# Performance work log

Measured on AMD Instinct MI355X. Metric: run time of the kernel, lower is better.

## Reference

```python
import jax, jax.numpy as jnp
import numpy as np

N = 65536      # n query/support points
NN = 34        # neighbors per point
K = 15         # kernel points
IN_F = 64
OUT_F = 64
RADIUS = 2.5
KP_EXTENT_CFG = 1.0
DENSITY = 5.0
EXTENT = KP_EXTENT_CFG * RADIUS / DENSITY  # effective KP_extent = 0.5
BN_EPS = 1e-6
LRELU_SLOPE = 0.1
POINT_DIM = 4  # modulated=True -> 3 offset dims + 1 modulation per kernel point


def make_kernel_points():
    # Deterministic stand-in for the precomputed kernel dispositions loaded
    # from disk in KPConv (fixed='center': first point at origin). Points lie
    # inside a ball of radius 1.5 * extent.
    rng = np.random.RandomState(42)
    kp = rng.normal(size=(K, 3))
    kp /= np.linalg.norm(kp, axis=1, keepdims=True)
    kp *= rng.uniform(0.3, 1.0, size=(K, 1))
    kp[0] = 0.0
    return jnp.asarray(kp * (1.5 * EXTENT), dtype=jnp.float32)


def setup_inputs() -> dict:
    key = jax.random.key(0)
    ks = jax.random.split(key, 8)
    query_points = jax.random.uniform(ks[0], (N, 3), dtype=jnp.float32)
    support_points = jax.random.uniform(ks[1], (N, 3), dtype=jnp.float32)
    neighbors_indices = jax.random.randint(ks[2], (N, NN), 0, N, dtype=jnp.int32)
    features = jax.random.normal(ks[3], (N, IN_F), dtype=jnp.float32)
    # weight_variable: truncated normal with std sqrt(2/size[-1])
    weight = jax.random.truncated_normal(ks[4], -2.0, 2.0, (K, IN_F, OUT_F), jnp.float32) * np.sqrt(2.0 / OUT_F)
    off_dim = POINT_DIM * K
    offset_weight = jax.random.truncated_normal(ks[5], -2.0, 2.0, (K, IN_F, off_dim), jnp.float32) * np.sqrt(2.0 / off_dim)
    offset_bias = jnp.zeros((off_dim,), jnp.float32)
    bn_gamma = jnp.ones((OUT_F,), jnp.float32)
    bn_beta = jnp.zeros((OUT_F,), jnp.float32)
    kernel_points = make_kernel_points()
    return dict(query_points=query_points, support_points=support_points,
                neighbors_indices=neighbors_indices, features=features,
                weight=weight, offset_weight=offset_weight, offset_bias=offset_bias,
                bn_gamma=bn_gamma, bn_beta=bn_beta, kernel_points=kernel_points)


def _influence(sq_dist):
    # KP_influence='linear': relu(1 - d / extent)
    return jax.nn.relu(1.0 - jnp.sqrt(sq_dist) / EXTENT)


def reference(query_points, support_points, neighbors_indices, features,
              weight, offset_weight, offset_bias, bn_gamma, bn_beta, kernel_points):
    n = query_points.shape[0]
    # Shadow point (far away) / shadow feature (zeros) appended at index n0
    supp_pad = jnp.concatenate([support_points, jnp.full((1, 3), 1e6, jnp.float32)], 0)
    feat_pad = jnp.concatenate([features, jnp.zeros((1, IN_F), jnp.float32)], 0)

    neigh_pts = supp_pad[neighbors_indices] - query_points[:, None, :]   # [n,nn,3]
    neigh_feats = feat_pad[neighbors_indices]                            # [n,nn,in]

    # ---- rigid KPConv producing per-point offsets (+ modulations) ----
    sq0 = jnp.sum((neigh_pts[:, :, None, :] - kernel_points[None, None]) ** 2, -1)  # [n,nn,K]
    w0 = _influence(sq0)
    wf0 = jnp.einsum('nak,nac->nkc', w0, neigh_feats)                    # [n,K,in]
    f0 = jnp.einsum('nkc,kcd->nd', wf0, offset_weight) + offset_bias     # [n,4K]
    offsets = f0[:, :3 * K].reshape(n, K, 3) * EXTENT                    # rescale to layer extent
    modulations = 2.0 * jax.nn.sigmoid(f0[:, 3 * K:])                    # [n,K]

    # ---- deformable KPConv ----
    def_kp = kernel_points[None] + offsets                               # [n,K,3]
    sq = jnp.sum((neigh_pts[:, :, None, :] - def_kp[:, None, :, :]) ** 2, -1)  # [n,nn,K]
    w = _influence(sq)                                                   # aggregation_mode='sum'
    wf = jnp.einsum('nak,nac->nkc', w, neigh_feats) * modulations[:, :, None]
    x = jnp.einsum('nkc,kco->no', wf, weight)                            # [n,out]

    # BatchNorm1d (training-mode batch stats, eps=1e-6) + LeakyReLU(0.1)
    mean = x.mean(0)
    var = x.var(0)
    x = (x - mean) * jax.lax.rsqrt(var + BN_EPS) * bn_gamma + bn_beta
    return jnp.where(x >= 0, x, LRELU_SLOPE * x)
```

## Files before the change

### kernel.cpp

```cpp
#include <hip/hip_runtime.h>
#include <math.h>

#define NPTS 65536

using half8   = __attribute__((ext_vector_type(8))) _Float16;
using half4   = __attribute__((ext_vector_type(4))) _Float16;
using floatx4 = __attribute__((ext_vector_type(4))) float;

__global__ __launch_bounds__(256) void k_prep(
    const float* __restrict__ ow, const float* __restrict__ w,
    const float* __restrict__ feat,
    _Float16* __restrict__ owt, _Float16* __restrict__ wt,
    _Float16* __restrict__ featH)
{
  int b = blockIdx.x;
  if (b < 256) {
    int i = b * 256 + threadIdx.x;
    int d = i >> 10, kc = i & 1023, c = kc >> 4, k = kc & 15;
    owt[i] = (k < 15 && d < 60) ? (_Float16)ow[(k * 64 + c) * 60 + d] : (_Float16)0.f;
    wt[i]  = (k < 15) ? (_Float16)w[(k * 64 + c) * 64 + d] : (_Float16)0.f;
  } else {
    int j = (b - 256) * 256 + threadIdx.x;
    float4 f = ((const float4*)feat)[j];
    half4 h = {(_Float16)f.x, (_Float16)f.y, (_Float16)f.z, (_Float16)f.w};
    ((half4*)featH)[j] = h;
  }
}

__global__ __launch_bounds__(256, 3) void k_fused(
    const float* __restrict__ query, const float* __restrict__ support,
    const int* __restrict__ nidx, const _Float16* __restrict__ featH,
    const float* __restrict__ kpts, const float* __restrict__ obias,
    const _Float16* __restrict__ owt, const _Float16* __restrict__ wt,
    float* __restrict__ outx)
{
  __shared__ float                  npx[16][34], npy[16][34], npz[16][34];
  __shared__ unsigned short         sidx[16][34];
  __shared__ __align__(16) _Float16 fT[4][64 * 32];
  __shared__ unsigned int           fx2[4][64];
  __shared__ __align__(16) _Float16 wfh[16 * 520];
  __shared__ float                  dk[16][64];

  const int tid  = threadIdx.x;
  const int wave = tid >> 6, lane = tid & 63;
  const int quad = lane >> 4, mm = lane & 15;
  const int base = blockIdx.x * 16;
  _Float16* fTw = fT[wave];
  unsigned int* fTw32 = (unsigned int*)fTw;
  unsigned int* fx2w = fx2[wave];
  const floatx4 fz = {0.f, 0.f, 0.f, 0.f};
  const int me = (mm < 15) ? mm : 14;

  for (int s = tid; s < 544; s += 256) {
    int pt = s / 34, a = s - pt * 34;
    int n = base + pt;
    int id = nidx[n * 34 + a];
    npx[pt][a] = support[id * 3 + 0] - query[n * 3 + 0];
    npy[pt][a] = support[id * 3 + 1] - query[n * 3 + 1];
    npz[pt][a] = support[id * 3 + 2] - query[n * 3 + 2];
    sidx[pt][a] = (unsigned short)id;
  }
  __syncthreads();

  auto load_g = [&](int pl, uint4* g0, uint4* g1) {
    #pragma unroll
    for (int it = 0; it < 3; ++it) {
      int task = it * 64 + lane;
      if (task < 136) {
        int rp = task >> 3, ch = task & 7;
        int i0 = (int)sidx[pl][2 * rp], i1 = (int)sidx[pl][2 * rp + 1];
        g0[it] = *(const uint4*)(featH + i0 * 64 + ch * 8);
        g1[it] = *(const uint4*)(featH + i1 * 64 + ch * 8);
      }
    }
  };
  auto transpose_g = [&](const uint4* g0, const uint4* g1) {
    #pragma unroll
    for (int it = 0; it < 3; ++it) {
      int task = it * 64 + lane;
      if (task < 136) {
        int rp = task >> 3, ch = task & 7;
        const uint* p0 = (const uint*)&g0[it];
        const uint* p1 = (const uint*)&g1[it];
        if (rp < 16) {
          int chunk = rp >> 2, o = rp & 3;
          #pragma unroll
          for (int cc = 0; cc < 8; ++cc) {
            int c  = ch * 8 + cc;
            int pc = chunk ^ ((ch ^ cc) & 3);
            uint v = __builtin_amdgcn_perm(p1[cc >> 1], p0[cc >> 1],
                                           (cc & 1) ? 0x07060302u : 0x05040100u);
            fTw32[c * 16 + pc * 4 + o] = v;
          }
        } else {
          #pragma unroll
          for (int cc = 0; cc < 8; ++cc) {
            uint v = __builtin_amdgcn_perm(p1[cc >> 1], p0[cc >> 1],
                                           (cc & 1) ? 0x07060302u : 0x05040100u);
            fx2w[ch * 8 + cc] = v;
          }
        }
      }
    }
  };

  auto conv_point = [&](int pl, float kx, float ky, float kz, const float* md,
                        floatx4* hold) {
    half8 a0;
    #pragma unroll
    for (int j = 0; j < 8; ++j) {
      int a = quad * 8 + j;
      float dx = npx[pl][a] - kx, dy = npy[pl][a] - ky, dz = npz[pl][a] - kz;
      float wv = 1.f - 2.f * sqrtf(dx * dx + dy * dy + dz * dz);
      a0[j] = (_Float16)fmaxf(wv, 0.f);
    }
    float w32, w33;
    {
      float dx = npx[pl][32] - kx, dy = npy[pl][32] - ky, dz = npz[pl][32] - kz;
      w32 = fmaxf(1.f - 2.f * sqrtf(dx * dx + dy * dy + dz * dz), 0.f);
      dx = npx[pl][33] - kx; dy = npy[pl][33] - ky; dz = npz[pl][33] - kz;
      w33 = fmaxf(1.f - 2.f * sqrtf(dx * dx + dy * dy + dz * dz), 0.f);
    }
    float w32r[4], w33r[4];
    #pragma unroll
    for (int r = 0; r < 4; ++r) {
      int src = (quad * 4 + r) << 2;
      w32r[r] = __int_as_float(__builtin_amdgcn_ds_bpermute(src, __float_as_int(w32)));
      w33r[r] = __int_as_float(__builtin_amdgcn_ds_bpermute(src, __float_as_int(w33)));
    }

    floatx4 acc[4];
    #pragma unroll
    for (int ct = 0; ct < 4; ++ct) {
      int c  = ct * 16 + mm;
      int pc = quad ^ (((c >> 3) ^ c) & 3);
      half8 b = *(const half8*)(fTw + c * 32 + pc * 8);
      acc[ct] = __builtin_amdgcn_mfma_f32_16x16x32_f16(a0, b, fz, 0, 0, 0);
    }
    #pragma unroll
    for (int ct = 0; ct < 4; ++ct) {
      int c = ct * 16 + mm;
      uint fp = fx2w[c];
      _Float16 lo = __builtin_bit_cast(_Float16, (unsigned short)(fp & 0xffffu));
      _Float16 hi = __builtin_bit_cast(_Float16, (unsigned short)(fp >> 16));
      float flo = (float)lo, fhi = (float)hi;
      #pragma unroll
      for (int r = 0; r < 4; ++r)
        acc[ct][r] = (acc[ct][r] + w32r[r] * flo + w33r[r] * fhi) * md[r];
    }

    _Float16* wp = wfh + pl * 520;
    #pragma unroll
    for (int ct = 0; ct < 2; ++ct) {
      half4 h = {(_Float16)acc[ct][0], (_Float16)acc[ct][1],
                 (_Float16)acc[ct][2], (_Float16)acc[ct][3]};
      *(half4*)(wp + (ct * 16 + mm) * 16 + quad * 4) = h;
    }
    hold[0] = acc[2]; hold[1] = acc[3];
  };

  auto write_hold = [&](const floatx4 (*hold)[2]) {
    #pragma unroll
    for (int pp = 0; pp < 4; ++pp) {
      _Float16* wp = wfh + (wave * 4 + pp) * 520;
      #pragma unroll
      for (int ct = 0; ct < 2; ++ct) {
        const floatx4& a = hold[pp][ct];
        half4 h = {(_Float16)a[0], (_Float16)a[1], (_Float16)a[2], (_Float16)a[3]};
        *(half4*)(wp + (ct * 16 + mm) * 16 + quad * 4) = h;
      }
    }
  };

  auto gemm_half = [&](const _Float16* bmat, int koff, floatx4& A, floatx4& B) {
    const _Float16* brow = bmat + (wave * 16 + mm) * 1024 + koff;
    const _Float16* arow = wfh + mm * 520;
    #pragma unroll
    for (int k2 = 0; k2 < 16; ++k2) {
      half8 af = *(const half8*)(arow + k2 * 32 + quad * 8);
      half8 bf = *(const half8*)(brow + k2 * 32 + quad * 8);
      if (k2 & 1) B = __builtin_amdgcn_mfma_f32_16x16x32_f16(af, bf, B, 0, 0, 0);
      else        A = __builtin_amdgcn_mfma_f32_16x16x32_f16(af, bf, A, 0, 0, 0);
    }
  };

  uint4 G0[2][3], G1[2][3];
  floatx4 hold[4][2];
  const float one4[4] = {1.f, 1.f, 1.f, 1.f};

  {
    float k0x = kpts[me * 3 + 0], k0y = kpts[me * 3 + 1], k0z = kpts[me * 3 + 2];
    load_g(wave * 4, G0[0], G1[0]);
    #pragma unroll
    for (int pp = 0; pp < 4; ++pp) {
      int pl = wave * 4 + pp;
      if (pp < 3) load_g(pl + 1, G0[(pp + 1) & 1], G1[(pp + 1) & 1]);
      transpose_g(G0[pp & 1], G1[pp & 1]);
      conv_point(pl, k0x, k0y, k0z, one4, hold[pp]);
    }
  }
  load_g(wave * 4, G0[0], G1[0]);
  __syncthreads();

  {
    floatx4 A = fz, B = fz;
    gemm_half(owt, 0, A, B);
    __syncthreads();
    write_hold(hold);
    __syncthreads();
    gemm_half(owt, 512, A, B);
    int d = wave * 16 + mm;
    float bv = (d < 60) ? obias[d] : 0.f;
    float kv = (d < 45) ? kpts[d] : 0.f;
    #pragma unroll
    for (int r = 0; r < 4; ++r) {
      int pt = quad * 4 + r;
      float v = A[r] + B[r] + bv;
      float o = (d < 45) ? (kv + 0.5f * v)
                         : (2.f / (1.f + expf(-v)));
      dk[pt][d] = o;
    }
  }
  __syncthreads();

  #pragma unroll
  for (int pp = 0; pp < 4; ++pp) {
    int pl = wave * 4 + pp;
    if (pp < 3) load_g(pl + 1, G0[(pp + 1) & 1], G1[(pp + 1) & 1]);
    float kx = dk[pl][me * 3 + 0], ky = dk[pl][me * 3 + 1], kz = dk[pl][me * 3 + 2];
    float md[4];
    #pragma unroll
    for (int r = 0; r < 4; ++r) {
      int k = quad * 4 + r;
      md[r] = (k < 15) ? dk[pl][45 + k] : 1.f;
    }
    transpose_g(G0[pp & 1], G1[pp & 1]);
    conv_point(pl, kx, ky, kz, md, hold[pp]);
  }
  __syncthreads();

  {
    floatx4 A = fz, B = fz;
    gemm_half(wt, 0, A, B);
    __syncthreads();
    write_hold(hold);
    __syncthreads();
    gemm_half(wt, 512, A, B);
    int d = wave * 16 + mm;
    #pragma unroll
    for (int r = 0; r < 4; ++r)
      outx[(base + quad * 4 + r) * 64 + d] = A[r] + B[r];
  }
}

__global__ __launch_bounds__(256) void k_stats(
    const float* __restrict__ x, float* __restrict__ stats)
{
  __shared__ float red[512];
  const int tid = threadIdx.x;
  const int c = tid & 63, g = tid >> 6;
  float s1 = 0.f, s2 = 0.f;
  for (int r = blockIdx.x * 4 + g; r < NPTS; r += 1024) {
    float v = x[r * 64 + c];
    s1 += v; s2 += v * v;
  }
  red[tid] = s1; red[256 + tid] = s2;
  __syncthreads();
  if (tid < 64) {
    s1 = red[tid] + red[tid + 64] + red[tid + 128] + red[tid + 192];
    s2 = red[256 + tid] + red[256 + tid + 64] + red[256 + tid + 128] + red[256 + tid + 192];
    atomicAdd(&stats[c], s1);
    atomicAdd(&stats[64 + c], s2);
  }
}

__global__ __launch_bounds__(256) void k_norm(
    float* __restrict__ x, const float* __restrict__ stats,
    const float* __restrict__ gamma, const float* __restrict__ beta)
{
  const int i = blockIdx.x * 256 + threadIdx.x;
  float4 v = ((float4*)x)[i];
  const int c0 = (i * 4) & 63;
  float o[4] = {v.x, v.y, v.z, v.w};
  #pragma unroll
  for (int j = 0; j < 4; ++j) {
    int c = c0 + j;
    float mean = stats[c] * (1.f / NPTS);
    float var  = stats[64 + c] * (1.f / NPTS) - mean * mean;
    float s = rsqrtf(var + 1e-6f) * gamma[c];
    float y = (o[j] - mean) * s + beta[c];
    o[j] = (y >= 0.f) ? y : 0.1f * y;
  }
  float4 rv = {o[0], o[1], o[2], o[3]};
  ((float4*)x)[i] = rv;
}

extern "C" void kernel_launch(void* const* d_in, const int* in_sizes, int n_in,
                              void* d_out, int out_size, void* d_ws, size_t ws_size,
                              hipStream_t stream)
{
  const float* query   = (const float*)d_in[0];
  const float* support = (const float*)d_in[1];
  const int*   nidx    = (const int*)d_in[2];
  const float* feat    = (const float*)d_in[3];
  const float* weight  = (const float*)d_in[4];
  const float* oweight = (const float*)d_in[5];
  const float* obias   = (const float*)d_in[6];
  const float* gamma   = (const float*)d_in[7];
  const float* beta    = (const float*)d_in[8];
  const float* kpts    = (const float*)d_in[9];
  float* x = (float*)d_out;

  char* ws = (char*)d_ws;
  _Float16* featH = (_Float16*)ws;
  _Float16* owt   = (_Float16*)(ws + 8388608);
  _Float16* wt    = (_Float16*)(ws + 8519680);
  float*    stats = (float*)(ws + 8650752);

  hipMemsetAsync(stats, 0, 512, stream);
  k_prep<<<4352, 256, 0, stream>>>(oweight, weight, feat, owt, wt, featH);
  k_fused<<<4096, 256, 0, stream>>>(query, support, nidx, featH, kpts, obias,
                                    owt, wt, x);
  k_stats<<<256, 256, 0, stream>>>(x, stats);
  k_norm<<<4096, 256, 0, stream>>>(x, stats, gamma, beta);
}
```

Before: 306.7 us.

## Shrink LDS staging to quarter tiles, fuse BN stats into main kernel

The weighted-feature staging buffer drops from half to quarter K-chunks, so the two GEMMs run in four stages and more accumulators are held in registers. LDS use falls, allowing launch bounds of 4 blocks per CU instead of 3. Neighbor offsets are packed as float4 with a precomputed squared norm, so distances come from a dot-product expansion. The fT layout is reswizzled. The separate stats kernel is removed: each block reduces its column sums with shuffles and adds them atomically, which costs more atomics and extra barriers.

```diff
diff --git a/kernel.cpp b/kernel.cpp
--- a/kernel.cpp
+++ b/kernel.cpp
@@ -27,19 +27,19 @@
   }
 }
 
-__global__ __launch_bounds__(256, 3) void k_fused(
+__global__ __launch_bounds__(256, 4) void k_fused(
     const float* __restrict__ query, const float* __restrict__ support,
     const int* __restrict__ nidx, const _Float16* __restrict__ featH,
     const float* __restrict__ kpts, const float* __restrict__ obias,
     const _Float16* __restrict__ owt, const _Float16* __restrict__ wt,
-    float* __restrict__ outx)
+    float* __restrict__ outx, float* __restrict__ stats)
 {
-  __shared__ float                  npx[16][34], npy[16][34], npz[16][34];
+  __shared__ float4                 np4[16][34];
   __shared__ unsigned short         sidx[16][34];
   __shared__ __align__(16) _Float16 fT[4][64 * 32];
   __shared__ unsigned int           fx2[4][64];
-  __shared__ __align__(16) _Float16 wfh[16 * 520];
-  __shared__ float                  dk[16][64];
+  __shared__ __align__(16) _Float16 wfh[16 * 264];
+  __shared__ float                  dk[16][60];
 
   const int tid  = threadIdx.x;
   const int wave = tid >> 6, lane = tid & 63;
@@ -55,9 +55,11 @@
     int pt = s / 34, a = s - pt * 34;
     int n = base + pt;
     int id = nidx[n * 34 + a];
-    npx[pt][a] = support[id * 3 + 0] - query[n * 3 + 0];
-    npy[pt][a] = support[id * 3 + 1] - query[n * 3 + 1];
-    npz[pt][a] = support[id * 3 + 2] - query[n * 3 + 2];
+    float dx = support[id * 3 + 0] - query[n * 3 + 0];
+    float dy = support[id * 3 + 1] - query[n * 3 + 1];
+    float dz = support[id * 3 + 2] - query[n * 3 + 2];
+    float4 q = {dx, dy, dz, dx * dx + dy * dy + dz * dz};
+    np4[pt][a] = q;
     sidx[pt][a] = (unsigned short)id;
   }
   __syncthreads();
@@ -87,10 +89,11 @@
           #pragma unroll
           for (int cc = 0; cc < 8; ++cc) {
             int c  = ch * 8 + cc;
-            int pc = chunk ^ ((ch ^ cc) & 3);
+            int f  = ((c & 7) << 3) | (c >> 3);
+            int pc = chunk ^ (((c >> 3) ^ c) & 3);
             uint v = __builtin_amdgcn_perm(p1[cc >> 1], p0[cc >> 1],
                                            (cc & 1) ? 0x07060302u : 0x05040100u);
-            fTw32[c * 16 + pc * 4 + o] = v;
+            fTw32[f * 16 + pc * 4 + o] = v;
           }
         } else {
           #pragma unroll
@@ -105,21 +108,26 @@
   };
 
   auto conv_point = [&](int pl, float kx, float ky, float kz, const float* md,
-                        floatx4* hold) {
+                        floatx4* hold3) {
+    float hk = kx * kx + ky * ky + kz * kz;
     half8 a0;
     #pragma unroll
     for (int j = 0; j < 8; ++j) {
       int a = quad * 8 + j;
-      float dx = npx[pl][a] - kx, dy = npy[pl][a] - ky, dz = npz[pl][a] - kz;
-      float wv = 1.f - 2.f * sqrtf(dx * dx + dy * dy + dz * dz);
+      float4 q = np4[pl][a];
+      float dt = q.x * kx + q.y * ky + q.z * kz;
+      float d2 = fmaxf(q.w + hk - 2.f * dt, 0.f);
+      float wv = 1.f - 2.f * sqrtf(d2);
       a0[j] = (_Float16)fmaxf(wv, 0.f);
     }
     float w32, w33;
     {
-      float dx = npx[pl][32] - kx, dy = npy[pl][32] - ky, dz = npz[pl][32] - kz;
-      w32 = fmaxf(1.f - 2.f * sqrtf(dx * dx + dy * dy + dz * dz), 0.f);
-      dx = npx[pl][33] - kx; dy = npy[pl][33] - ky; dz = npz[pl][33] - kz;
-      w33 = fmaxf(1.f - 2.f * sqrtf(dx * dx + dy * dy + dz * dz), 0.f);
+      float4 q = np4[pl][32];
+      float dt = q.x * kx + q.y * ky + q.z * kz;
+      w32 = fmaxf(1.f - 2.f * sqrtf(fmaxf(q.w + hk - 2.f * dt, 0.f)), 0.f);
+      q = np4[pl][33];
+      dt = q.x * kx + q.y * ky + q.z * kz;
+      w33 = fmaxf(1.f - 2.f * sqrtf(fmaxf(q.w + hk - 2.f * dt, 0.f)), 0.f);
     }
     float w32r[4], w33r[4];
     #pragma unroll
@@ -133,8 +141,9 @@
     #pragma unroll
     for (int ct = 0; ct < 4; ++ct) {
       int c  = ct * 16 + mm;
+      int f  = ((c & 7) << 3) | (c >> 3);
       int pc = quad ^ (((c >> 3) ^ c) & 3);
-      half8 b = *(const half8*)(fTw + c * 32 + pc * 8);
+      half8 b = *(const half8*)(fTw + f * 32 + pc * 8);
       acc[ct] = __builtin_amdgcn_mfma_f32_16x16x32_f16(a0, b, fz, 0, 0, 0);
     }
     #pragma unroll
@@ -149,34 +158,27 @@
         acc[ct][r] = (acc[ct][r] + w32r[r] * flo + w33r[r] * fhi) * md[r];
     }
 
-    _Float16* wp = wfh + pl * 520;
-    #pragma unroll
-    for (int ct = 0; ct < 2; ++ct) {
-      half4 h = {(_Float16)acc[ct][0], (_Float16)acc[ct][1],
-                 (_Float16)acc[ct][2], (_Float16)acc[ct][3]};
-      *(half4*)(wp + (ct * 16 + mm) * 16 + quad * 4) = h;
-    }
-    hold[0] = acc[2]; hold[1] = acc[3];
-  };
-
-  auto write_hold = [&](const floatx4 (*hold)[2]) {
+    _Float16* wp = wfh + pl * 264;
+    half4 h = {(_Float16)acc[0][0], (_Float16)acc[0][1],
+               (_Float16)acc[0][2], (_Float16)acc[0][3]};
+    *(half4*)(wp + mm * 16 + quad * 4) = h;
+    hold3[0] = acc[1]; hold3[1] = acc[2]; hold3[2] = acc[3];
+  };
+
+  auto write_hold = [&](const floatx4 (*hold)[3], int idx) {
     #pragma unroll
     for (int pp = 0; pp < 4; ++pp) {
-      _Float16* wp = wfh + (wave * 4 + pp) * 520;
-      #pragma unroll
-      for (int ct = 0; ct < 2; ++ct) {
-        const floatx4& a = hold[pp][ct];
-        half4 h = {(_Float16)a[0], (_Float16)a[1], (_Float16)a[2], (_Float16)a[3]};
-        *(half4*)(wp + (ct * 16 + mm) * 16 + quad * 4) = h;
-      }
-    }
-  };
-
-  auto gemm_half = [&](const _Float16* bmat, int koff, floatx4& A, floatx4& B) {
-    const _Float16* brow = bmat + (wave * 16 + mm) * 1024 + koff;
-    const _Float16* arow = wfh + mm * 520;
-    #pragma unroll
-    for (int k2 = 0; k2 < 16; ++k2) {
+      const floatx4& a = hold[pp][idx];
+      half4 h = {(_Float16)a[0], (_Float16)a[1], (_Float16)a[2], (_Float16)a[3]};
+      *(half4*)(wfh + (wave * 4 + pp) * 264 + mm * 16 + quad * 4) = h;
+    }
+  };
+
+  auto gemm_q = [&](const _Float16* bmat, int p, floatx4& A, floatx4& B) {
+    const _Float16* brow = bmat + (wave * 16 + mm) * 1024 + p * 256;
+    const _Float16* arow = wfh + mm * 264;
+    #pragma unroll
+    for (int k2 = 0; k2 < 8; ++k2) {
       half8 af = *(const half8*)(arow + k2 * 32 + quad * 8);
       half8 bf = *(const half8*)(brow + k2 * 32 + quad * 8);
       if (k2 & 1) B = __builtin_amdgcn_mfma_f32_16x16x32_f16(af, bf, B, 0, 0, 0);
@@ -185,7 +187,7 @@
   };
 
   uint4 G0[2][3], G1[2][3];
-  floatx4 hold[4][2];
+  floatx4 hold[4][3];
   const float one4[4] = {1.f, 1.f, 1.f, 1.f};
 
   {
@@ -204,11 +206,13 @@
 
   {
     floatx4 A = fz, B = fz;
-    gemm_half(owt, 0, A, B);
-    __syncthreads();
-    write_hold(hold);
-    __syncthreads();
-    gemm_half(owt, 512, A, B);
+    gemm_q(owt, 0, A, B);
+    __syncthreads(); write_hold(hold, 0); __syncthreads();
+    gemm_q(owt, 1, A, B);
+    __syncthreads(); write_hold(hold, 1); __syncthreads();
+    gemm_q(owt, 2, A, B);
+    __syncthreads(); write_hold(hold, 2); __syncthreads();
+    gemm_q(owt, 3, A, B);
     int d = wave * 16 + mm;
     float bv = (d < 60) ? obias[d] : 0.f;
     float kv = (d < 45) ? kpts[d] : 0.f;
@@ -216,9 +220,9 @@
     for (int r = 0; r < 4; ++r) {
       int pt = quad * 4 + r;
       float v = A[r] + B[r] + bv;
-      float o = (d < 45) ? (kv + 0.5f * v)
-                         : (2.f / (1.f + expf(-v)));
-      dk[pt][d] = o;
+      if (d < 60)
+        dk[pt][d] = (d < 45) ? (kv + 0.5f * v)
+                             : (2.f / (1.f + expf(-v)));
     }
   }
   __syncthreads();
@@ -232,7 +236,9 @@
     #pragma unroll
     for (int r = 0; r < 4; ++r) {
       int k = quad * 4 + r;
-      md[r] = (k < 15) ? dk[pl][45 + k] : 1.f;
+      int kk = (k < 15) ? k : 14;
+      float t = dk[pl][45 + kk];
+      md[r] = (k < 15) ? t : 1.f;
     }
     transpose_g(G0[pp & 1], G1[pp & 1]);
     conv_point(pl, kx, ky, kz, md, hold[pp]);
@@ -241,36 +247,27 @@
 
   {
     floatx4 A = fz, B = fz;
-    gemm_half(wt, 0, A, B);
-    __syncthreads();
-    write_hold(hold);
-    __syncthreads();
-    gemm_half(wt, 512, A, B);
+    gemm_q(wt, 0, A, B);
+    __syncthreads(); write_hold(hold, 0); __syncthreads();
+    gemm_q(wt, 1, A, B);
+    __syncthreads(); write_hold(hold, 1); __syncthreads();
+    gemm_q(wt, 2, A, B);
+    __syncthreads(); write_hold(hold, 2); __syncthreads();
+    gemm_q(wt, 3, A, B);
     int d = wave * 16 + mm;
-    #pragma unroll
-    for (int r = 0; r < 4; ++r)
-      outx[(base + quad * 4 + r) * 64 + d] = A[r] + B[r];
-  }
-}
-
-__global__ __launch_bounds__(256) void k_stats(
-    const float* __restrict__ x, float* __restrict__ stats)
-{
-  __shared__ float red[512];
-  const int tid = threadIdx.x;
-  const int c = tid & 63, g = tid >> 6;
-  float s1 = 0.f, s2 = 0.f;
-  for (int r = blockIdx.x * 4 + g; r < NPTS; r += 1024) {
-    float v = x[r * 64 + c];
-    s1 += v; s2 += v * v;
-  }
-  red[tid] = s1; red[256 + tid] = s2;
-  __syncthreads();
-  if (tid < 64) {
-    s1 = red[tid] + red[tid + 64] + red[tid + 128] + red[tid + 192];
-    s2 = red[256 + tid] + red[256 + tid + 64] + red[256 + tid + 128] + red[256 + tid + 192];
-    atomicAdd(&stats[c], s1);
-    atomicAdd(&stats[64 + c], s2);
+    float s1 = 0.f, s2 = 0.f;
+    #pragma unroll
+    for (int r = 0; r < 4; ++r) {
+      float v = A[r] + B[r];
+      outx[(base + quad * 4 + r) * 64 + d] = v;
+      s1 += v; s2 += v * v;
+    }
+    s1 += __shfl_xor(s1, 16); s2 += __shfl_xor(s2, 16);
+    s1 += __shfl_xor(s1, 32); s2 += __shfl_xor(s2, 32);
+    if (lane < 16) {
+      atomicAdd(&stats[d], s1);
+      atomicAdd(&stats[64 + d], s2);
+    }
   }
 }
 
@@ -320,7 +317,6 @@
   hipMemsetAsync(stats, 0, 512, stream);
   k_prep<<<4352, 256, 0, stream>>>(oweight, weight, feat, owt, wt, featH);
   k_fused<<<4096, 256, 0, stream>>>(query, support, nidx, featH, kpts, obias,
-                                    owt, wt, x);
-  k_stats<<<256, 256, 0, stream>>>(x, stats);
+                                    owt, wt, x, stats);
   k_norm<<<4096, 256, 0, stream>>>(x, stats, gamma, beta);
 }
```

Result: slower. 465.3 us (+51.7%).
